# Performance work log

Hardware: AMD Instinct MI355X
Metric: run time of the kernel (lower is better)

The kernel has to match this reference:

```python
import jax, jax.numpy as jnp
import numpy as np

N_NODES = 100000
N_EDGES = 3200000
D_IN = 256
D_OUT = 256


def setup_inputs() -> dict:
    key = jax.random.key(0)
    k1, k2, k3, k4, k5 = jax.random.split(key, 5)
    x = jax.random.normal(k1, (N_NODES, D_IN), dtype=jnp.float32)
    edge_row = jax.random.randint(k2, (N_EDGES,), 0, N_NODES, dtype=jnp.int32)
    edge_col = jax.random.randint(k3, (N_EDGES,), 0, N_NODES, dtype=jnp.int32)
    edge_val = jax.random.uniform(k4, (N_EDGES,), dtype=jnp.float32)
    # Linear weight [out_dim, in_dim], kaiming-uniform-like scale
    bound = 1.0 / np.sqrt(D_IN)
    W = jax.random.uniform(k5, (D_OUT, D_IN), dtype=jnp.float32,
                           minval=-bound, maxval=bound)
    return {"x": x, "edge_row": edge_row, "edge_col": edge_col,
            "edge_val": edge_val, "W": W}


def reference(x, edge_row, edge_col, edge_val, W):
    # SpMM: agg[i] = sum_{edges e with row=i} val_e * x[col_e]
    msgs = edge_val[:, None] * x[edge_col]            # [E, D_IN] gather
    agg = jax.ops.segment_sum(msgs, edge_row, num_segments=N_NODES)  # [N, D_IN]
    # Dense linear projection (bias=False): agg @ W.T
    return agg @ W.T                                  # [N, D_OUT]
```

## Files before the change

kernel.cpp:

```cpp
#include <hip/hip_runtime.h>
#include <hip/hip_bf16.h>
#include <stdint.h>

#define N_NODES 100000
#define N_EDGES 3200000
#define D_FEAT 256
#define NBKT 782
#define RPB 128
#define CHUNK 8192
#define NBLK_E 391
#define CAP 6144

typedef __attribute__((ext_vector_type(8))) short short8;
typedef __attribute__((ext_vector_type(8))) ushort ushort8;
typedef __attribute__((ext_vector_type(4))) float float4v;

__device__ inline unsigned short f2bf(float f) {
    union { float f; unsigned u; } v; v.f = f;
    unsigned u = v.u;
    u += 0x7FFF + ((u >> 16) & 1);
    return (unsigned short)(u >> 16);
}
__device__ inline float bf2f(unsigned short u) {
    union { unsigned u; float f; } v; v.u = (unsigned)u << 16;
    return v.f;
}

__global__ __launch_bounds__(256) void xconv_kernel(const float4* __restrict__ x4,
                                                    ushort4* __restrict__ xbf4) {
    int i = blockIdx.x * 256 + threadIdx.x;
    float4 v = x4[i];
    ushort4 o;
    o.x = f2bf(v.x); o.y = f2bf(v.y); o.z = f2bf(v.z); o.w = f2bf(v.w);
    xbf4[i] = o;
}


__global__ __launch_bounds__(256) void coarse_hist(const int* __restrict__ erow,
                                                   int* __restrict__ hist) {
    __shared__ int cnt[NBKT];
    for (int b = threadIdx.x; b < NBKT; b += 256) cnt[b] = 0;
    __syncthreads();
    int cb = blockIdx.x * CHUNK;
    for (int j = 0; j < CHUNK; j += 256) {
        int i = cb + j + threadIdx.x;
        if (i < N_EDGES) atomicAdd(&cnt[erow[i] >> 7], 1);
    }
    __syncthreads();
    for (int b = threadIdx.x; b < NBKT; b += 256)
        hist[blockIdx.x * NBKT + b] = cnt[b];
}

__global__ __launch_bounds__(512) void scan_blocks(int* __restrict__ hist,
                                                   int* __restrict__ totals) {
    __shared__ int s[512];
    int b = blockIdx.x;
    int t = threadIdx.x;
    int v = (t < NBLK_E) ? hist[t * NBKT + b] : 0;
    s[t] = v;
    __syncthreads();
    for (int o = 1; o < 512; o <<= 1) {
        int x = (t >= o) ? s[t - o] : 0;
        __syncthreads();
        s[t] += x;
        __syncthreads();
    }
    if (t < NBLK_E) hist[t * NBKT + b] = s[t] - v;
    if (t == NBLK_E - 1) totals[b] = s[t];
}

__global__ __launch_bounds__(1024) void scan_buckets(const int* __restrict__ totals,
                                                     int* __restrict__ base_) {
    __shared__ int s[1024];
    int t = threadIdx.x;
    int v = (t < NBKT) ? totals[t] : 0;
    s[t] = v;
    __syncthreads();
    for (int o = 1; o < 1024; o <<= 1) {
        int x = (t >= o) ? s[t - o] : 0;
        __syncthreads();
        s[t] += x;
        __syncthreads();
    }
    if (t < NBKT) base_[t] = s[t] - v;
    if (t == 0) base_[NBKT] = N_EDGES;
}

__global__ __launch_bounds__(256) void coarse_scatter(
        const int* __restrict__ erow, const int* __restrict__ ecol,
        const float* __restrict__ eval,
        const int* __restrict__ hist, const int* __restrict__ base_,
        uint2* __restrict__ tmp) {
    __shared__ int lbase[NBKT];
    __shared__ int cnt[NBKT];
    for (int b = threadIdx.x; b < NBKT; b += 256) {
        lbase[b] = hist[blockIdx.x * NBKT + b] + base_[b];
        cnt[b] = 0;
    }
    __syncthreads();
    int cb = blockIdx.x * CHUNK;
    for (int j = 0; j < CHUNK; j += 256) {
        int i = cb + j + threadIdx.x;
        if (i < N_EDGES) {
            int r = erow[i];
            int b = r >> 7;
            int pos = lbase[b] + atomicAdd(&cnt[b], 1);
            uint2 cv;
            cv.x = (unsigned)ecol[i] | ((unsigned)(r & 127) << 17);
            union { float f; unsigned u; } w; w.f = eval[i];
            cv.y = w.u;
            tmp[pos] = cv;
        }
    }
}

__global__ __launch_bounds__(512) void spmm_fused(
        const ushort* __restrict__ xbf,
        const uint2* __restrict__ tmp,
        const int* __restrict__ base_,
        ushort* __restrict__ agg_bf) {
    __shared__ uint2 ed[CAP];
    __shared__ int cnt[RPB];
    __shared__ int excl[RPB];
    __shared__ int cur[RPB];
    int b = blockIdx.x;
    int t = threadIdx.x;
    int s0 = base_[b];
    int nb = base_[b + 1] - s0;

    if (t < RPB) cnt[t] = 0;
    __syncthreads();
    for (int j = t; j < nb; j += 512)
        atomicAdd(&cnt[(tmp[s0 + j].x >> 17) & 127], 1);
    __syncthreads();
    if (t < RPB) excl[t] = cnt[t];
    __syncthreads();
    for (int o = 1; o < RPB; o <<= 1) {
        int x = (t < RPB && t >= o) ? excl[t - o] : 0;
        __syncthreads();
        if (t < RPB) excl[t] += x;
        __syncthreads();
    }
    if (t < RPB) { int ex = excl[t] - cnt[t]; excl[t] = ex; cur[t] = ex; }
    __syncthreads();
    for (int j = t; j < nb; j += 512) {
        uint2 cv = tmp[s0 + j];
        unsigned rl = (cv.x >> 17) & 127;
        int dst = atomicAdd(&cur[rl], 1);
        ed[dst] = cv;
    }
    __syncthreads();

    int wv   = t >> 6;
    int lane = t & 63;
    int half = lane >> 5;
    int hl   = lane & 31;
    for (int rl = wv; rl < RPB; rl += 8) {
        int row = b * RPB + rl;
        if (row >= N_NODES) break;
        int sE = excl[rl];
        int eE = sE + cnt[rl];
        float acc[8] = {0.f, 0.f, 0.f, 0.f, 0.f, 0.f, 0.f, 0.f};
        int e = sE + half;
        for (; e + 6 < eE; e += 8) {
            uint2 c0 = ed[e];
            uint2 c1 = ed[e + 2];
            uint2 c2 = ed[e + 4];
            uint2 c3 = ed[e + 6];
            ushort8 v0 = *(const ushort8*)&xbf[(size_t)(c0.x & 0x1FFFF) * 256 + hl * 8];
            ushort8 v1 = *(const ushort8*)&xbf[(size_t)(c1.x & 0x1FFFF) * 256 + hl * 8];
            ushort8 v2 = *(const ushort8*)&xbf[(size_t)(c2.x & 0x1FFFF) * 256 + hl * 8];
            ushort8 v3 = *(const ushort8*)&xbf[(size_t)(c3.x & 0x1FFFF) * 256 + hl * 8];
            union { unsigned u; float f; } w0, w1, w2, w3;
            w0.u = c0.y; w1.u = c1.y; w2.u = c2.y; w3.u = c3.y;
            #pragma unroll
            for (int j = 0; j < 8; ++j) acc[j] += w0.f * bf2f(v0[j]);
            #pragma unroll
            for (int j = 0; j < 8; ++j) acc[j] += w1.f * bf2f(v1[j]);
            #pragma unroll
            for (int j = 0; j < 8; ++j) acc[j] += w2.f * bf2f(v2[j]);
            #pragma unroll
            for (int j = 0; j < 8; ++j) acc[j] += w3.f * bf2f(v3[j]);
        }
        for (; e < eE; e += 2) {
            uint2 cv = ed[e];
            ushort8 v = *(const ushort8*)&xbf[(size_t)(cv.x & 0x1FFFF) * 256 + hl * 8];
            union { unsigned u; float f; } w; w.u = cv.y;
            #pragma unroll
            for (int j = 0; j < 8; ++j) acc[j] += w.f * bf2f(v[j]);
        }
        #pragma unroll
        for (int j = 0; j < 8; ++j) acc[j] += __shfl_xor(acc[j], 32, 64);
        if (half == 0) {
            ushort8 o;
            #pragma unroll
            for (int j = 0; j < 8; ++j) o[j] = f2bf(acc[j]);
            *(ushort8*)&agg_bf[(size_t)row * 256 + hl * 8] = o;
        }
    }
}

__global__ void wconv_kernel(const float* __restrict__ W, ushort* __restrict__ Wbf) {
    int i = blockIdx.x * 256 + threadIdx.x;
    Wbf[i] = f2bf(W[i]);
}

__global__ __launch_bounds__(256) void gemm_kernel(
        const ushort* __restrict__ Abf,
        const ushort* __restrict__ Wbf,
        float* __restrict__ out) {
    int w    = threadIdx.x >> 6;
    int lane = threadIdx.x & 63;
    int quad = lane >> 4;
    int l16  = lane & 15;
    int rt   = blockIdx.x * 64;

    float4v acc[4][4];
    #pragma unroll
    for (int mt = 0; mt < 4; ++mt)
        #pragma unroll
        for (int nt = 0; nt < 4; ++nt) acc[mt][nt] = (float4v){0.f, 0.f, 0.f, 0.f};

    #pragma unroll
    for (int k0 = 0; k0 < 256; k0 += 32) {
        short8 a[4], bf[4];
        #pragma unroll
        for (int mt = 0; mt < 4; ++mt) {
            int row = rt + mt * 16 + l16;
            if (row >= N_NODES) row = N_NODES - 1;
            a[mt] = *(const short8*)&Abf[(size_t)row * 256 + k0 + quad * 8];
        }
        #pragma unroll
        for (int nt = 0; nt < 4; ++nt) {
            int n = w * 64 + nt * 16 + l16;
            bf[nt] = *(const short8*)&Wbf[n * 256 + k0 + quad * 8];
        }
        #pragma unroll
        for (int mt = 0; mt < 4; ++mt)
            #pragma unroll
            for (int nt = 0; nt < 4; ++nt)
                acc[mt][nt] = __builtin_amdgcn_mfma_f32_16x16x32_bf16(a[mt], bf[nt], acc[mt][nt], 0, 0, 0);
    }
    #pragma unroll
    for (int mt = 0; mt < 4; ++mt)
        #pragma unroll
        for (int nt = 0; nt < 4; ++nt) {
            int n = w * 64 + nt * 16 + l16;
            #pragma unroll
            for (int r = 0; r < 4; ++r) {
                int row = rt + mt * 16 + quad * 4 + r;
                if (row < N_NODES) out[(size_t)row * 256 + n] = acc[mt][nt][r];
            }
        }
}


extern "C" void kernel_launch(void* const* d_in, const int* in_sizes, int n_in,
                              void* d_out, int out_size, void* d_ws, size_t ws_size,
                              hipStream_t stream) {
    const float* x    = (const float*)d_in[0];
    const int*   erow = (const int*)d_in[1];
    const int*   ecol = (const int*)d_in[2];
    const float* eval = (const float*)d_in[3];
    const float* W    = (const float*)d_in[4];
    float* out = (float*)d_out;

    char* ws = (char*)d_ws;
    size_t off = 0;
    int* hist      = (int*)(ws + off);   off += ((size_t)NBLK_E * NBKT * 4 + 255) & ~255ull;
    int* totals    = (int*)(ws + off);   off += ((size_t)NBKT * 4 + 255) & ~255ull;
    int* base_     = (int*)(ws + off);   off += ((size_t)(NBKT + 1) * 4 + 255) & ~255ull;
    uint2* tmp_cv  = (uint2*)(ws + off); off += (size_t)N_EDGES * 8;
    ushort* Wbf    = (ushort*)(ws + off);  off += (size_t)D_FEAT * D_FEAT * 2;
    ushort* xbf    = (ushort*)(ws + off);  off += (size_t)N_NODES * D_FEAT * 2;
    ushort* agg_bf = (ushort*)(ws + off);  off += (size_t)N_NODES * D_FEAT * 2;

    xconv_kernel<<<(N_NODES * D_FEAT / 4) / 256, 256, 0, stream>>>((const float4*)x, (ushort4*)xbf);
    coarse_hist<<<NBLK_E, 256, 0, stream>>>(erow, hist);
    scan_blocks<<<NBKT, 512, 0, stream>>>(hist, totals);
    scan_buckets<<<1, 1024, 0, stream>>>(totals, base_);
    coarse_scatter<<<NBLK_E, 256, 0, stream>>>(erow, ecol, eval, hist, base_, tmp_cv);
    wconv_kernel<<<(D_FEAT * D_FEAT) / 256, 256, 0, stream>>>(W, Wbf);
    spmm_fused<<<NBKT, 512, 0, stream>>>(xbf, tmp_cv, base_, agg_bf);
    gemm_kernel<<<(N_NODES + 63) / 64, 256, 0, stream>>>(agg_bf, Wbf, out);
}
```

Baseline: 609.9 us.

## Split fused bucket sort+SpMM into fine-sort kernel and row-parallel SpMM kernel

The fused kernel, which sorted each 128-row bucket in LDS and then aggregated it, becomes two kernels. A fine_sort kernel writes a global CSR array plus row_start offsets, and a new SpMM kernel assigns one wavefront per row across many small blocks. The coarse pass also uses smaller chunks (more blocks), and the block scan now handles 4 entries per thread. The split is meant to lift occupancy in the SpMM, which was limited by the large LDS staging buffer, at the cost of an extra 25.6MB write and read of sorted edges plus one more kernel launch.

```diff
diff --git a/kernel.cpp b/kernel.cpp
--- a/kernel.cpp
+++ b/kernel.cpp
@@ -7,9 +7,8 @@
 #define D_FEAT 256
 #define NBKT 782
 #define RPB 128
-#define CHUNK 8192
-#define NBLK_E 391
-#define CAP 6144
+#define CHUNK 2048
+#define NBLK_E 1563
 
 typedef __attribute__((ext_vector_type(8))) short short8;
 typedef __attribute__((ext_vector_type(8))) ushort ushort8;
@@ -42,6 +41,7 @@
     for (int b = threadIdx.x; b < NBKT; b += 256) cnt[b] = 0;
     __syncthreads();
     int cb = blockIdx.x * CHUNK;
+    #pragma unroll
     for (int j = 0; j < CHUNK; j += 256) {
         int i = cb + j + threadIdx.x;
         if (i < N_EDGES) atomicAdd(&cnt[erow[i] >> 7], 1);
@@ -56,8 +56,15 @@
     __shared__ int s[512];
     int b = blockIdx.x;
     int t = threadIdx.x;
-    int v = (t < NBLK_E) ? hist[t * NBKT + b] : 0;
-    s[t] = v;
+    int v[4];
+    int sum = 0;
+    #pragma unroll
+    for (int j = 0; j < 4; ++j) {
+        int c = t * 4 + j;
+        v[j] = (c < NBLK_E) ? hist[c * NBKT + b] : 0;
+        sum += v[j];
+    }
+    s[t] = sum;
     __syncthreads();
     for (int o = 1; o < 512; o <<= 1) {
         int x = (t >= o) ? s[t - o] : 0;
@@ -65,12 +72,18 @@
         s[t] += x;
         __syncthreads();
     }
-    if (t < NBLK_E) hist[t * NBKT + b] = s[t] - v;
-    if (t == NBLK_E - 1) totals[b] = s[t];
+    int run = s[t] - sum;
+    #pragma unroll
+    for (int j = 0; j < 4; ++j) {
+        int c = t * 4 + j;
+        if (c < NBLK_E) { hist[c * NBKT + b] = run; run += v[j]; }
+    }
+    if (t == 511) totals[b] = run;
 }
 
 __global__ __launch_bounds__(1024) void scan_buckets(const int* __restrict__ totals,
-                                                     int* __restrict__ base_) {
+                                                     int* __restrict__ base_,
+                                                     int* __restrict__ row_start) {
     __shared__ int s[1024];
     int t = threadIdx.x;
     int v = (t < NBKT) ? totals[t] : 0;
@@ -83,7 +96,7 @@
         __syncthreads();
     }
     if (t < NBKT) base_[t] = s[t] - v;
-    if (t == 0) base_[NBKT] = N_EDGES;
+    if (t == 0) { base_[NBKT] = N_EDGES; row_start[N_NODES] = N_EDGES; }
 }
 
 __global__ __launch_bounds__(256) void coarse_scatter(
@@ -99,6 +112,7 @@
     }
     __syncthreads();
     int cb = blockIdx.x * CHUNK;
+    #pragma unroll
     for (int j = 0; j < CHUNK; j += 256) {
         int i = cb + j + threadIdx.x;
         if (i < N_EDGES) {
@@ -114,12 +128,10 @@
     }
 }
 
-__global__ __launch_bounds__(512) void spmm_fused(
-        const ushort* __restrict__ xbf,
-        const uint2* __restrict__ tmp,
-        const int* __restrict__ base_,
-        ushort* __restrict__ agg_bf) {
-    __shared__ uint2 ed[CAP];
+__global__ __launch_bounds__(512) void fine_sort(const uint2* __restrict__ tmp,
+                                                 const int* __restrict__ base_,
+                                                 uint2* __restrict__ csr,
+                                                 int* __restrict__ row_start) {
     __shared__ int cnt[RPB];
     __shared__ int excl[RPB];
     __shared__ int cur[RPB];
@@ -127,7 +139,6 @@
     int t = threadIdx.x;
     int s0 = base_[b];
     int nb = base_[b + 1] - s0;
-
     if (t < RPB) cnt[t] = 0;
     __syncthreads();
     for (int j = t; j < nb; j += 512)
@@ -141,62 +152,70 @@
         if (t < RPB) excl[t] += x;
         __syncthreads();
     }
-    if (t < RPB) { int ex = excl[t] - cnt[t]; excl[t] = ex; cur[t] = ex; }
+    if (t < RPB) {
+        int ex = excl[t] - cnt[t];
+        excl[t] = ex;
+        cur[t] = ex;
+        int row = b * RPB + t;
+        if (row < N_NODES) row_start[row] = s0 + ex;
+    }
     __syncthreads();
     for (int j = t; j < nb; j += 512) {
         uint2 cv = tmp[s0 + j];
         unsigned rl = (cv.x >> 17) & 127;
-        int dst = atomicAdd(&cur[rl], 1);
-        ed[dst] = cv;
-    }
-    __syncthreads();
-
-    int wv   = t >> 6;
-    int lane = t & 63;
+        int dst = s0 + atomicAdd(&cur[rl], 1);
+        csr[dst] = cv;
+    }
+}
+
+__global__ __launch_bounds__(256) void spmm_kernel(
+        const ushort* __restrict__ xbf,
+        const int* __restrict__ row_start,
+        const uint2* __restrict__ csr_cv,
+        ushort* __restrict__ agg_bf) {
+    int row  = (blockIdx.x * blockDim.x + threadIdx.x) >> 6;
+    int lane = threadIdx.x & 63;
     int half = lane >> 5;
     int hl   = lane & 31;
-    for (int rl = wv; rl < RPB; rl += 8) {
-        int row = b * RPB + rl;
-        if (row >= N_NODES) break;
-        int sE = excl[rl];
-        int eE = sE + cnt[rl];
-        float acc[8] = {0.f, 0.f, 0.f, 0.f, 0.f, 0.f, 0.f, 0.f};
-        int e = sE + half;
-        for (; e + 6 < eE; e += 8) {
-            uint2 c0 = ed[e];
-            uint2 c1 = ed[e + 2];
-            uint2 c2 = ed[e + 4];
-            uint2 c3 = ed[e + 6];
-            ushort8 v0 = *(const ushort8*)&xbf[(size_t)(c0.x & 0x1FFFF) * 256 + hl * 8];
-            ushort8 v1 = *(const ushort8*)&xbf[(size_t)(c1.x & 0x1FFFF) * 256 + hl * 8];
-            ushort8 v2 = *(const ushort8*)&xbf[(size_t)(c2.x & 0x1FFFF) * 256 + hl * 8];
-            ushort8 v3 = *(const ushort8*)&xbf[(size_t)(c3.x & 0x1FFFF) * 256 + hl * 8];
-            union { unsigned u; float f; } w0, w1, w2, w3;
-            w0.u = c0.y; w1.u = c1.y; w2.u = c2.y; w3.u = c3.y;
-            #pragma unroll
-            for (int j = 0; j < 8; ++j) acc[j] += w0.f * bf2f(v0[j]);
-            #pragma unroll
-            for (int j = 0; j < 8; ++j) acc[j] += w1.f * bf2f(v1[j]);
-            #pragma unroll
-            for (int j = 0; j < 8; ++j) acc[j] += w2.f * bf2f(v2[j]);
-            #pragma unroll
-            for (int j = 0; j < 8; ++j) acc[j] += w3.f * bf2f(v3[j]);
-        }
-        for (; e < eE; e += 2) {
-            uint2 cv = ed[e];
-            ushort8 v = *(const ushort8*)&xbf[(size_t)(cv.x & 0x1FFFF) * 256 + hl * 8];
-            union { unsigned u; float f; } w; w.u = cv.y;
-            #pragma unroll
-            for (int j = 0; j < 8; ++j) acc[j] += w.f * bf2f(v[j]);
-        }
-        #pragma unroll
-        for (int j = 0; j < 8; ++j) acc[j] += __shfl_xor(acc[j], 32, 64);
-        if (half == 0) {
-            ushort8 o;
-            #pragma unroll
-            for (int j = 0; j < 8; ++j) o[j] = f2bf(acc[j]);
-            *(ushort8*)&agg_bf[(size_t)row * 256 + hl * 8] = o;
-        }
+    if (row >= N_NODES) return;
+    int start = row_start[row];
+    int end   = row_start[row + 1];
+    float acc[8] = {0.f, 0.f, 0.f, 0.f, 0.f, 0.f, 0.f, 0.f};
+    int e = start + half;
+    for (; e + 6 < end; e += 8) {
+        uint2 c0 = csr_cv[e];
+        uint2 c1 = csr_cv[e + 2];
+        uint2 c2 = csr_cv[e + 4];
+        uint2 c3 = csr_cv[e + 6];
+        ushort8 v0 = *(const ushort8*)&xbf[(size_t)(c0.x & 0x1FFFF) * 256 + hl * 8];
+        ushort8 v1 = *(const ushort8*)&xbf[(size_t)(c1.x & 0x1FFFF) * 256 + hl * 8];
+        ushort8 v2 = *(const ushort8*)&xbf[(size_t)(c2.x & 0x1FFFF) * 256 + hl * 8];
+        ushort8 v3 = *(const ushort8*)&xbf[(size_t)(c3.x & 0x1FFFF) * 256 + hl * 8];
+        union { unsigned u; float f; } w0, w1, w2, w3;
+        w0.u = c0.y; w1.u = c1.y; w2.u = c2.y; w3.u = c3.y;
+        #pragma unroll
+        for (int j = 0; j < 8; ++j) acc[j] += w0.f * bf2f(v0[j]);
+        #pragma unroll
+        for (int j = 0; j < 8; ++j) acc[j] += w1.f * bf2f(v1[j]);
+        #pragma unroll
+        for (int j = 0; j < 8; ++j) acc[j] += w2.f * bf2f(v2[j]);
+        #pragma unroll
+        for (int j = 0; j < 8; ++j) acc[j] += w3.f * bf2f(v3[j]);
+    }
+    for (; e < end; e += 2) {
+        uint2 cv = csr_cv[e];
+        ushort8 v = *(const ushort8*)&xbf[(size_t)(cv.x & 0x1FFFF) * 256 + hl * 8];
+        union { unsigned u; float f; } w; w.u = cv.y;
+        #pragma unroll
+        for (int j = 0; j < 8; ++j) acc[j] += w.f * bf2f(v[j]);
+    }
+    #pragma unroll
+    for (int j = 0; j < 8; ++j) acc[j] += __shfl_xor(acc[j], 32, 64);
+    if (half == 0) {
+        ushort8 o;
+        #pragma unroll
+        for (int j = 0; j < 8; ++j) o[j] = f2bf(acc[j]);
+        *(ushort8*)&agg_bf[(size_t)row * 256 + hl * 8] = o;
     }
 }
 
@@ -270,7 +289,9 @@
     int* hist      = (int*)(ws + off);   off += ((size_t)NBLK_E * NBKT * 4 + 255) & ~255ull;
     int* totals    = (int*)(ws + off);   off += ((size_t)NBKT * 4 + 255) & ~255ull;
     int* base_     = (int*)(ws + off);   off += ((size_t)(NBKT + 1) * 4 + 255) & ~255ull;
+    int* row_start = (int*)(ws + off);   off += ((size_t)(N_NODES + 1) * 4 + 255) & ~255ull;
     uint2* tmp_cv  = (uint2*)(ws + off); off += (size_t)N_EDGES * 8;
+    uint2* csr_cv  = (uint2*)(ws + off); off += (size_t)N_EDGES * 8;
     ushort* Wbf    = (ushort*)(ws + off);  off += (size_t)D_FEAT * D_FEAT * 2;
     ushort* xbf    = (ushort*)(ws + off);  off += (size_t)N_NODES * D_FEAT * 2;
     ushort* agg_bf = (ushort*)(ws + off);  off += (size_t)N_NODES * D_FEAT * 2;
@@ -278,9 +299,10 @@
     xconv_kernel<<<(N_NODES * D_FEAT / 4) / 256, 256, 0, stream>>>((const float4*)x, (ushort4*)xbf);
     coarse_hist<<<NBLK_E, 256, 0, stream>>>(erow, hist);
     scan_blocks<<<NBKT, 512, 0, stream>>>(hist, totals);
-    scan_buckets<<<1, 1024, 0, stream>>>(totals, base_);
+    scan_buckets<<<1, 1024, 0, stream>>>(totals, base_, row_start);
     coarse_scatter<<<NBLK_E, 256, 0, stream>>>(erow, ecol, eval, hist, base_, tmp_cv);
+    fine_sort<<<NBKT, 512, 0, stream>>>(tmp_cv, base_, csr_cv, row_start);
     wconv_kernel<<<(D_FEAT * D_FEAT) / 256, 256, 0, stream>>>(W, Wbf);
-    spmm_fused<<<NBKT, 512, 0, stream>>>(xbf, tmp_cv, base_, agg_bf);
+    spmm_kernel<<<N_NODES / 4, 256, 0, stream>>>(xbf, row_start, csr_cv, agg_bf);
     gemm_kernel<<<(N_NODES + 63) / 64, 256, 0, stream>>>(agg_bf, Wbf, out);
 }
```

Measured after the change: 598.6 us. No clear change (-1.9%).
